# Performance work log

Measured on AMD Instinct MI355X. Metric: run time of the kernel, lower is better.

## Reference

```python
import jax, jax.numpy as jnp
import numpy as np

N, D, B, E, K, H, C = 100000, 256, 20000, 16, 3, 256, 40  # m = K = 3


def setup_inputs() -> dict:
    key = jax.random.key(0)
    ks = jax.random.split(key, 11)
    return {
        "nodes": jax.random.randint(ks[0], (B,), 0, N, dtype=jnp.int32),
        "structure": jax.random.randint(ks[1], (B, E, K), 0, N, dtype=jnp.int32),
        "X": jax.random.normal(ks[2], (N, D), dtype=jnp.float32),
        "beta": jax.random.uniform(ks[3], (1,), dtype=jnp.float32),
        "w_att_w": jax.random.normal(ks[4], (1,), dtype=jnp.float32),
        "w_att_b": jax.random.normal(ks[5], (1,), dtype=jnp.float32),
        "lin_W": jax.random.normal(ks[6], (H, D), dtype=jnp.float32) * 0.05,
        "lin_b": jax.random.normal(ks[7], (H,), dtype=jnp.float32) * 0.05,
        "skip_W": jax.random.normal(ks[8], (H, D), dtype=jnp.float32) * 0.05,
        "cls_W": jax.random.normal(ks[9], (C, H), dtype=jnp.float32) * 0.05,
        "cls_b": jax.random.normal(ks[10], (C,), dtype=jnp.float32) * 0.05,
    }


def reference(nodes, structure, X, beta, w_att_w, w_att_b, lin_W, lin_b, skip_W, cls_W, cls_b):
    # --- TMessagePassing (batched over nodes and hyperedges) ---
    feats = X[structure]                                  # [B, E, K, D] gather
    # variance over nodes in the hyperedge (unbiased=False), mean over feature dim
    edge_var = jnp.var(feats, axis=2).mean(axis=-1)       # [B, E]
    att = jax.nn.sigmoid(w_att_w[0] * edge_var + w_att_b[0])  # [B, E]
    # len(edge) == m (K == m=3): msg = prod(feats[:-1], dim=0)
    msg = jnp.prod(feats[:, :, : K - 1, :], axis=2)       # [B, E, D]
    neigh = jnp.einsum("be,bed->bd", att, msg)            # sum of att * msg over edges
    # --- Encoder (combine == 'sum') ---
    self_feat = X[nodes]                                  # [B, D]
    h = self_feat + neigh
    enc = jax.nn.relu(h @ lin_W.T + lin_b)                # [B, H]
    enc = (1.0 - beta[0]) * enc + beta[0] * (self_feat @ skip_W.T)
    # --- classifier + log_softmax ---
    logits = enc @ cls_W.T + cls_b                        # [B, C]
    return jax.nn.log_softmax(logits, axis=1)
```

## Files before the change

kernel.cpp:

```cpp
#include <hip/hip_runtime.h>
#include <hip/hip_bf16.h>
#include <math.h>

#define Dn 256
#define En 16
#define Kn 3
#define Hn 256
#define Cn 40
#define CnP 48

typedef __attribute__((ext_vector_type(8)))  short bf16x8;
typedef __attribute__((ext_vector_type(4)))  float f32x4;

static __device__ __forceinline__ float bf2f(unsigned short u) {
    return __uint_as_float(((unsigned)u) << 16);
}
static __device__ __forceinline__ unsigned short f2bfbits(float v) {
    __hip_bfloat16 hb = __float2bfloat16(v);
    return *reinterpret_cast<unsigned short*>(&hb);
}
static __device__ __forceinline__ unsigned pack2bf(float a, float b) {
    return (unsigned)f2bfbits(a) | ((unsigned)f2bfbits(b) << 16);
}
static __device__ __forceinline__ unsigned swz4(unsigned boff) {
    return boff ^ (((boff >> 9) & 15u) << 4);
}

__global__ __launch_bounds__(256) void conv_all(
    const float* __restrict__ X, const float* __restrict__ linW,
    const float* __restrict__ skipW, const float* __restrict__ clsW,
    uint4* __restrict__ Xb, uint4* __restrict__ linWp,
    uint4* __restrict__ skipWp, uint4* __restrict__ clsWp,
    int x8, int w8)
{
    int t = blockIdx.x * 256 + threadIdx.x;
    const int c8 = (CnP * Hn) / 8;
    if (t < x8) {
        const float4* iv = reinterpret_cast<const float4*>(X);
        const float4 a = iv[(size_t)t * 2 + 0];
        const float4 b = iv[(size_t)t * 2 + 1];
        Xb[t] = (uint4){pack2bf(a.x, a.y), pack2bf(a.z, a.w),
                        pack2bf(b.x, b.y), pack2bf(b.z, b.w)};
        return;
    }
    t -= x8;
    if (t < w8) {
        const float4* iv = reinterpret_cast<const float4*>(linW);
        const float4 a = iv[(size_t)t * 2 + 0];
        const float4 b = iv[(size_t)t * 2 + 1];
        const int lc = (t >> 5) & 15, ct = t >> 9;
        const int kt = (t >> 2) & 7,  kg = t & 3;
        linWp[(ct * 8 + kt) * 64 + kg * 16 + lc] =
            (uint4){pack2bf(a.x, a.y), pack2bf(a.z, a.w),
                    pack2bf(b.x, b.y), pack2bf(b.z, b.w)};
        return;
    }
    t -= w8;
    if (t < w8) {
        const float4* iv = reinterpret_cast<const float4*>(skipW);
        const float4 a = iv[(size_t)t * 2 + 0];
        const float4 b = iv[(size_t)t * 2 + 1];
        const int lc = (t >> 5) & 15, ct = t >> 9;
        const int kt = (t >> 2) & 7,  kg = t & 3;
        skipWp[(ct * 8 + kt) * 64 + kg * 16 + lc] =
            (uint4){pack2bf(a.x, a.y), pack2bf(a.z, a.w),
                    pack2bf(b.x, b.y), pack2bf(b.z, b.w)};
        return;
    }
    t -= w8;
    if (t < c8) {
        const int col = t >> 5;
        const int lc = col & 15, ct = t >> 9;
        const int kt = (t >> 2) & 7, kg = t & 3;
        const int dst = (ct * 8 + kt) * 64 + kg * 16 + lc;
        if (col < Cn) {
            const float4* iv = reinterpret_cast<const float4*>(clsW);
            const float4 a = iv[(size_t)t * 2 + 0];
            const float4 b = iv[(size_t)t * 2 + 1];
            clsWp[dst] = (uint4){pack2bf(a.x, a.y), pack2bf(a.z, a.w),
                                 pack2bf(b.x, b.y), pack2bf(b.z, b.w)};
        } else {
            clsWp[dst] = (uint4){0u, 0u, 0u, 0u};
        }
    }
}

__global__ __launch_bounds__(256) void mp_kernel_bf(
    const int* __restrict__ nodes, const int* __restrict__ structure,
    const uint2* __restrict__ Xb,
    const float* __restrict__ waw_p, const float* __restrict__ wab_p,
    uint2* __restrict__ h_out, uint2* __restrict__ self_out, int B)
{
    const int wave = threadIdx.x >> 6;
    const int lane = threadIdx.x & 63;
    const int b = blockIdx.x * 4 + wave;
    if (b >= B) return;
    const int ub = __builtin_amdgcn_readfirstlane(b);

    const float waw = waw_p[0];
    const float wab = wab_p[0];

    float4 neigh = make_float4(0.f, 0.f, 0.f, 0.f);
    const int* st = structure + (size_t)ub * (En * Kn);

    #pragma unroll 1
    for (int g = 0; g < En / 4; ++g) {
        int idx[12];
        #pragma unroll
        for (int u = 0; u < 12; ++u) idx[u] = st[g * 12 + u];

        uint2 r0[4], r1[4], r2[4];
        #pragma unroll
        for (int u = 0; u < 4; ++u) {
            r0[u] = Xb[(size_t)idx[u * 3 + 0] * (Dn / 4) + lane];
            r1[u] = Xb[(size_t)idx[u * 3 + 1] * (Dn / 4) + lane];
            r2[u] = Xb[(size_t)idx[u * 3 + 2] * (Dn / 4) + lane];
        }

        float pv[4];
        float4 msg[4];
        #pragma unroll
        for (int u = 0; u < 4; ++u) {
            float4 f0, f1, f2;
            f0.x = bf2f((unsigned short)(r0[u].x & 0xffff));
            f0.y = bf2f((unsigned short)(r0[u].x >> 16));
            f0.z = bf2f((unsigned short)(r0[u].y & 0xffff));
            f0.w = bf2f((unsigned short)(r0[u].y >> 16));
            f1.x = bf2f((unsigned short)(r1[u].x & 0xffff));
            f1.y = bf2f((unsigned short)(r1[u].x >> 16));
            f1.z = bf2f((unsigned short)(r1[u].y & 0xffff));
            f1.w = bf2f((unsigned short)(r1[u].y >> 16));
            f2.x = bf2f((unsigned short)(r2[u].x & 0xffff));
            f2.y = bf2f((unsigned short)(r2[u].x >> 16));
            f2.z = bf2f((unsigned short)(r2[u].y & 0xffff));
            f2.w = bf2f((unsigned short)(r2[u].y >> 16));

            float s2 = 0.f, cr = 0.f, tt;
            s2 = fmaf(f0.x, f0.x, s2); s2 = fmaf(f1.x, f1.x, s2); s2 = fmaf(f2.x, f2.x, s2);
            tt = f1.x + f2.x; cr = fmaf(f0.x, tt, cr); cr = fmaf(f1.x, f2.x, cr);
            s2 = fmaf(f0.y, f0.y, s2); s2 = fmaf(f1.y, f1.y, s2); s2 = fmaf(f2.y, f2.y, s2);
            tt = f1.y + f2.y; cr = fmaf(f0.y, tt, cr); cr = fmaf(f1.y, f2.y, cr);
            s2 = fmaf(f0.z, f0.z, s2); s2 = fmaf(f1.z, f1.z, s2); s2 = fmaf(f2.z, f2.z, s2);
            tt = f1.z + f2.z; cr = fmaf(f0.z, tt, cr); cr = fmaf(f1.z, f2.z, cr);
            s2 = fmaf(f0.w, f0.w, s2); s2 = fmaf(f1.w, f1.w, s2); s2 = fmaf(f2.w, f2.w, s2);
            tt = f1.w + f2.w; cr = fmaf(f0.w, tt, cr); cr = fmaf(f1.w, f2.w, cr);

            pv[u] = s2 - cr;
            msg[u].x = f0.x * f1.x;
            msg[u].y = f0.y * f1.y;
            msg[u].z = f0.z * f1.z;
            msg[u].w = f0.w * f1.w;
        }

        #pragma unroll
        for (int off = 32; off; off >>= 1) {
            #pragma unroll
            for (int u = 0; u < 4; ++u) pv[u] += __shfl_xor(pv[u], off);
        }

        #pragma unroll
        for (int u = 0; u < 4; ++u) {
            const float var_mean = pv[u] * (2.f / (9.f * (float)Dn));
            const float att = 1.f / (1.f + expf(-(waw * var_mean + wab)));
            neigh.x += att * msg[u].x;
            neigh.y += att * msg[u].y;
            neigh.z += att * msg[u].z;
            neigh.w += att * msg[u].w;
        }
    }

    const uint2 sv = Xb[(size_t)nodes[ub] * (Dn / 4) + lane];
    self_out[(size_t)b * (Dn / 4) + lane] = sv;
    const float sx = bf2f((unsigned short)(sv.x & 0xffff));
    const float sy = bf2f((unsigned short)(sv.x >> 16));
    const float sz = bf2f((unsigned short)(sv.y & 0xffff));
    const float sw = bf2f((unsigned short)(sv.y >> 16));
    uint2 o;
    o.x = pack2bf(sx + neigh.x, sy + neigh.y);
    o.y = pack2bf(sz + neigh.z, sw + neigh.w);
    h_out[(size_t)b * (Dn / 4) + lane] = o;
}

__global__ __launch_bounds__(256, 4) void enc_cls16(
    const unsigned short* __restrict__ hB,
    const unsigned short* __restrict__ selfB,
    const uint4* __restrict__ linWp, const float* __restrict__ linb,
    const uint4* __restrict__ skipWp, const float* __restrict__ beta_p,
    const uint4* __restrict__ clsWp,
    const float* __restrict__ clsb,
    float* __restrict__ out, int M)
{
    __shared__ unsigned short hlds[16 * 256];
    __shared__ unsigned short slds[16 * 256];
    __shared__ unsigned short elds[16 * 256];

    const int w    = threadIdx.x >> 6;
    const int l    = threadIdx.x & 63;
    const int lr16 = l & 15;
    const int kg   = l >> 4;
    const int row0 = blockIdx.x * 16;

    #pragma unroll
    for (int it = 0; it < 2; ++it) {
        const int ch = it * 256 + threadIdx.x;
        const int r  = ch >> 5;
        const int c  = ch & 31;
        int grow = row0 + r;
        grow = grow < M ? grow : (M - 1);
        const uint4 hv = *reinterpret_cast<const uint4*>(hB    + (size_t)grow * Dn + c * 8);
        const uint4 sv = *reinterpret_cast<const uint4*>(selfB + (size_t)grow * Dn + c * 8);
        const unsigned boff = swz4((unsigned)(r * 512 + c * 16));
        *reinterpret_cast<uint4*>(reinterpret_cast<char*>(hlds) + boff) = hv;
        *reinterpret_cast<uint4*>(reinterpret_cast<char*>(slds) + boff) = sv;
    }
    __syncthreads();

    f32x4 acc1[4], acc2[4];
    #pragma unroll
    for (int n = 0; n < 4; ++n) {
        acc1[n] = (f32x4){0.f, 0.f, 0.f, 0.f};
        acc2[n] = (f32x4){0.f, 0.f, 0.f, 0.f};
    }

    #pragma unroll 2
    for (int k0 = 0; k0 < Dn; k0 += 32) {
        const int kt = k0 >> 5;
        const unsigned aoff = swz4((unsigned)(lr16 * 512 + k0 * 2 + kg * 16));
        const bf16x8 a1 = *reinterpret_cast<const bf16x8*>(
            reinterpret_cast<const char*>(hlds) + aoff);
        const bf16x8 a2 = *reinterpret_cast<const bf16x8*>(
            reinterpret_cast<const char*>(slds) + aoff);
        #pragma unroll
        for (int n = 0; n < 4; ++n) {
            const int fidx = ((w * 4 + n) * 8 + kt) * 64 + l;
            const bf16x8 b1 = *reinterpret_cast<const bf16x8*>(linWp  + fidx);
            const bf16x8 b2 = *reinterpret_cast<const bf16x8*>(skipWp + fidx);
            acc1[n] = __builtin_amdgcn_mfma_f32_16x16x32_bf16(a1, b1, acc1[n], 0, 0, 0);
            acc2[n] = __builtin_amdgcn_mfma_f32_16x16x32_bf16(a2, b2, acc2[n], 0, 0, 0);
        }
    }

    const float beta = beta_p[0];
    const float omb = 1.f - beta;
    #pragma unroll
    for (int n = 0; n < 4; ++n) {
        const int col = w * 64 + n * 16 + lr16;
        const float bias = linb[col];
        #pragma unroll
        for (int r = 0; r < 4; ++r) {
            const int rowl = kg * 4 + r;
            const float c1 = fmaxf(acc1[n][r] + bias, 0.f);
            const unsigned short v = f2bfbits(omb * c1 + beta * acc2[n][r]);
            const unsigned boff = swz4((unsigned)(rowl * 512 + col * 2));
            *reinterpret_cast<unsigned short*>(
                reinterpret_cast<char*>(elds) + boff) = v;
        }
    }
    __syncthreads();

    if (w == 0) {
        f32x4 cacc[3];
        cacc[0] = (f32x4){0.f,0.f,0.f,0.f};
        cacc[1] = (f32x4){0.f,0.f,0.f,0.f};
        cacc[2] = (f32x4){0.f,0.f,0.f,0.f};

        #pragma unroll
        for (int k0 = 0; k0 < Hn; k0 += 32) {
            const int kt = k0 >> 5;
            const unsigned boff = swz4((unsigned)(lr16 * 512 + k0 * 2 + kg * 16));
            const bf16x8 a = *reinterpret_cast<const bf16x8*>(
                reinterpret_cast<const char*>(elds) + boff);
            #pragma unroll
            for (int t = 0; t < 3; ++t) {
                const bf16x8 bb = *reinterpret_cast<const bf16x8*>(
                    clsWp + ((t * 8 + kt) * 64 + l));
                cacc[t] = __builtin_amdgcn_mfma_f32_16x16x32_bf16(a, bb, cacc[t], 0, 0, 0);
            }
        }

        float bias3[3];
        #pragma unroll
        for (int t = 0; t < 3; ++t) {
            const int cb = t * 16 + lr16;
            bias3[t] = (cb < Cn) ? clsb[cb] : -INFINITY;
        }

        #pragma unroll
        for (int r = 0; r < 4; ++r) {
            float lg0 = cacc[0][r] + bias3[0];
            float lg1 = cacc[1][r] + bias3[1];
            float lg2 = cacc[2][r] + bias3[2];
            float mx = fmaxf(fmaxf(lg0, lg1), lg2);
            #pragma unroll
            for (int off = 8; off; off >>= 1) mx = fmaxf(mx, __shfl_xor(mx, off));
            float se = expf(lg0 - mx) + expf(lg1 - mx) + expf(lg2 - mx);
            #pragma unroll
            for (int off = 8; off; off >>= 1) se += __shfl_xor(se, off);
            const float lse = logf(se);

            const int row = row0 + kg * 4 + r;
            if (row < M) {
                if (lr16 < 8) out[(size_t)row * Cn + 32 + lr16] = lg2 - mx - lse;
                out[(size_t)row * Cn + lr16]      = lg0 - mx - lse;
                out[(size_t)row * Cn + 16 + lr16] = lg1 - mx - lse;
            }
        }
    }
}

__global__ __launch_bounds__(256) void mp_kernel_f32(
    const int* __restrict__ nodes, const int* __restrict__ structure,
    const float* __restrict__ X, const float* __restrict__ waw_p,
    const float* __restrict__ wab_p, float* __restrict__ h_out, int B)
{
    const int wave = threadIdx.x >> 6;
    const int lane = threadIdx.x & 63;
    const int b = blockIdx.x * 4 + wave;
    if (b >= B) return;
    const int ub = __builtin_amdgcn_readfirstlane(b);

    const float waw = waw_p[0];
    const float wab = wab_p[0];
    const float4* __restrict__ Xv = reinterpret_cast<const float4*>(X);

    float4 neigh = make_float4(0.f, 0.f, 0.f, 0.f);
    const int* st = structure + (size_t)ub * (En * Kn);

    #pragma unroll 1
    for (int e = 0; e < En; ++e) {
        const int i0 = st[e * 3 + 0];
        const int i1 = st[e * 3 + 1];
        const int i2 = st[e * 3 + 2];
        const float4 f0 = Xv[(size_t)i0 * (Dn / 4) + lane];
        const float4 f1 = Xv[(size_t)i1 * (Dn / 4) + lane];
        const float4 f2 = Xv[(size_t)i2 * (Dn / 4) + lane];
        float pv = 0.f;
        {
            float a, bb, c, m;
            a = f0.x; bb = f1.x; c = f2.x;
            m = (a + bb + c) * (1.f / 3.f);
            pv += (a * a + bb * bb + c * c) * (1.f / 3.f) - m * m;
            a = f0.y; bb = f1.y; c = f2.y;
            m = (a + bb + c) * (1.f / 3.f);
            pv += (a * a + bb * bb + c * c) * (1.f / 3.f) - m * m;
            a = f0.z; bb = f1.z; c = f2.z;
            m = (a + bb + c) * (1.f / 3.f);
            pv += (a * a + bb * bb + c * c) * (1.f / 3.f) - m * m;
            a = f0.w; bb = f1.w; c = f2.w;
            m = (a + bb + c) * (1.f / 3.f);
            pv += (a * a + bb * bb + c * c) * (1.f / 3.f) - m * m;
        }
        #pragma unroll
        for (int off = 32; off; off >>= 1) pv += __shfl_xor(pv, off);
        const float var_mean = pv * (1.f / (float)Dn);
        const float att = 1.f / (1.f + expf(-(waw * var_mean + wab)));
        neigh.x += att * f0.x * f1.x;
        neigh.y += att * f0.y * f1.y;
        neigh.z += att * f0.z * f1.z;
        neigh.w += att * f0.w * f1.w;
    }

    const float4 s = Xv[(size_t)nodes[ub] * (Dn / 4) + lane];
    float4 h;
    h.x = s.x + neigh.x; h.y = s.y + neigh.y;
    h.z = s.z + neigh.z; h.w = s.w + neigh.w;
    reinterpret_cast<float4*>(h_out)[(size_t)b * (Dn / 4) + lane] = h;
}

#define BM 64
#define BN 64
#define BKs 16
#define LDT 68

__global__ __launch_bounds__(256) void enc_gemm_f32(
    const float* __restrict__ hA, const int* __restrict__ nodes,
    const float* __restrict__ X,
    const float* __restrict__ linW, const float* __restrict__ linb,
    const float* __restrict__ skipW, const float* __restrict__ beta_p,
    float* __restrict__ enc2, int M)
{
    __shared__ float Ats1[BKs][LDT];
    __shared__ float Ats2[BKs][LDT];
    __shared__ float Bts1[BKs][LDT];
    __shared__ float Bts2[BKs][LDT];

    const int tid = threadIdx.x;
    const int tx = tid & 15;
    const int ty = tid >> 4;
    const int row0 = blockIdx.x * BM;
    const int col0 = blockIdx.y * BN;

    const int lr = tid >> 2;
    const int lc = tid & 3;

    const int arow = row0 + lr;
    const bool arow_ok = arow < M;
    const int self_row = arow_ok ? nodes[arow] : 0;

    float acc1[4][4] = {{0.f}}, acc2[4][4] = {{0.f}};

    for (int k0 = 0; k0 < Dn; k0 += BKs) {
        float4 a1v = make_float4(0.f, 0.f, 0.f, 0.f);
        float4 a2v = make_float4(0.f, 0.f, 0.f, 0.f);
        if (arow_ok) {
            a1v = *reinterpret_cast<const float4*>(hA + (size_t)arow * Dn + k0 + lc * 4);
            a2v = *reinterpret_cast<const float4*>(X + (size_t)self_row * Dn + k0 + lc * 4);
        }
        const float4 b1v = *reinterpret_cast<const float4*>(linW + (size_t)(col0 + lr) * Dn + k0 + lc * 4);
        const float4 b2v = *reinterpret_cast<const float4*>(skipW + (size_t)(col0 + lr) * Dn + k0 + lc * 4);

        __syncthreads();
        Ats1[lc * 4 + 0][lr] = a1v.x; Ats1[lc * 4 + 1][lr] = a1v.y;
        Ats1[lc * 4 + 2][lr] = a1v.z; Ats1[lc * 4 + 3][lr] = a1v.w;
        Ats2[lc * 4 + 0][lr] = a2v.x; Ats2[lc * 4 + 1][lr] = a2v.y;
        Ats2[lc * 4 + 2][lr] = a2v.z; Ats2[lc * 4 + 3][lr] = a2v.w;
        Bts1[lc * 4 + 0][lr] = b1v.x; Bts1[lc * 4 + 1][lr] = b1v.y;
        Bts1[lc * 4 + 2][lr] = b1v.z; Bts1[lc * 4 + 3][lr] = b1v.w;
        Bts2[lc * 4 + 0][lr] = b2v.x; Bts2[lc * 4 + 1][lr] = b2v.y;
        Bts2[lc * 4 + 2][lr] = b2v.z; Bts2[lc * 4 + 3][lr] = b2v.w;
        __syncthreads();

        #pragma unroll
        for (int kk = 0; kk < BKs; ++kk) {
            const float4 a1 = *reinterpret_cast<const float4*>(&Ats1[kk][ty * 4]);
            const float4 a2 = *reinterpret_cast<const float4*>(&Ats2[kk][ty * 4]);
            const float4 b1 = *reinterpret_cast<const float4*>(&Bts1[kk][tx * 4]);
            const float4 b2 = *reinterpret_cast<const float4*>(&Bts2[kk][tx * 4]);
            const float a1a[4] = {a1.x, a1.y, a1.z, a1.w};
            const float a2a[4] = {a2.x, a2.y, a2.z, a2.w};
            const float b1a[4] = {b1.x, b1.y, b1.z, b1.w};
            const float b2a[4] = {b2.x, b2.y, b2.z, b2.w};
            #pragma unroll
            for (int i = 0; i < 4; ++i)
                #pragma unroll
                for (int j = 0; j < 4; ++j) {
                    acc1[i][j] = fmaf(a1a[i], b1a[j], acc1[i][j]);
                    acc2[i][j] = fmaf(a2a[i], b2a[j], acc2[i][j]);
                }
        }
    }

    const float beta = beta_p[0];
    const float omb = 1.f - beta;
    #pragma unroll
    for (int i = 0; i < 4; ++i) {
        const int r = row0 + ty * 4 + i;
        if (r >= M) continue;
        #pragma unroll
        for (int j = 0; j < 4; ++j) {
            const int c = col0 + tx * 4 + j;
            float c1 = acc1[i][j] + linb[c];
            c1 = fmaxf(c1, 0.f);
            enc2[(size_t)r * Hn + c] = omb * c1 + beta * acc2[i][j];
        }
    }
}

__global__ __launch_bounds__(256) void cls_kernel_f32(
    const float* __restrict__ enc2, const float* __restrict__ clsW,
    const float* __restrict__ clsb, float* __restrict__ out, int B)
{
    const int wave = threadIdx.x >> 6;
    const int lane = threadIdx.x & 63;
    const int b = blockIdx.x * 4 + wave;
    if (b >= B) return;

    const float4 e = reinterpret_cast<const float4*>(enc2 + (size_t)b * Hn)[lane];
    const float4* __restrict__ clsWv = reinterpret_cast<const float4*>(clsW);

    float mylogit = -INFINITY;
    #pragma unroll
    for (int c0 = 0; c0 < Cn; c0 += 8) {
        float p[8];
        #pragma unroll
        for (int u = 0; u < 8; ++u) {
            const float4 wv = clsWv[(size_t)(c0 + u) * (Hn / 4) + lane];
            p[u] = e.x * wv.x + e.y * wv.y + e.z * wv.z + e.w * wv.w;
        }
        #pragma unroll
        for (int off = 32; off; off >>= 1) {
            #pragma unroll
            for (int u = 0; u < 8; ++u) p[u] += __shfl_xor(p[u], off);
        }
        #pragma unroll
        for (int u = 0; u < 8; ++u)
            if (lane == c0 + u) mylogit = p[u];
    }
    if (lane < Cn) mylogit += clsb[lane];

    float mx = mylogit;
    #pragma unroll
    for (int off = 32; off; off >>= 1) mx = fmaxf(mx, __shfl_xor(mx, off));
    float ex = (lane < Cn) ? expf(mylogit - mx) : 0.f;
    float se = ex;
    #pragma unroll
    for (int off = 32; off; off >>= 1) se += __shfl_xor(se, off);
    const float lse = logf(se);

    if (lane < Cn) out[(size_t)b * Cn + lane] = mylogit - mx - lse;
}

extern "C" void kernel_launch(void* const* d_in, const int* in_sizes, int n_in,
                              void* d_out, int out_size, void* d_ws, size_t ws_size,
                              hipStream_t stream) {
    const int*   nodes     = (const int*)d_in[0];
    const int*   structure = (const int*)d_in[1];
    const float* X         = (const float*)d_in[2];
    const float* beta      = (const float*)d_in[3];
    const float* waw       = (const float*)d_in[4];
    const float* wab       = (const float*)d_in[5];
    const float* linW      = (const float*)d_in[6];
    const float* linb      = (const float*)d_in[7];
    const float* skipW     = (const float*)d_in[8];
    const float* clsW      = (const float*)d_in[9];
    const float* clsb      = (const float*)d_in[10];
    float* out = (float*)d_out;

    const int B = in_sizes[0];
    const int Ntot = in_sizes[2];

    unsigned short* h_bf   = (unsigned short*)d_ws;
    unsigned short* selfb  = h_bf + (size_t)B * Dn;
    unsigned short* Xb     = selfb + (size_t)B * Dn;
    unsigned short* linWp  = Xb + (size_t)Ntot;
    unsigned short* skipWp = linWp + (size_t)Hn * Dn;
    unsigned short* clsWp  = skipWp + (size_t)Hn * Dn;

    const size_t need = ((size_t)B * Dn * 2 + (size_t)Ntot +
                         (size_t)Hn * Dn * 2 + (size_t)CnP * Hn) * 2;

    if (ws_size >= need) {
        const int x8 = Ntot / 8;
        const int w8 = (Hn * Dn) / 8;
        const int c8 = (CnP * Hn) / 8;
        const int G = x8 + 2 * w8 + c8;
        conv_all<<<(G + 255) / 256, 256, 0, stream>>>(
            X, linW, skipW, clsW,
            (uint4*)Xb, (uint4*)linWp, (uint4*)skipWp, (uint4*)clsWp, x8, w8);

        mp_kernel_bf<<<(B + 3) / 4, 256, 0, stream>>>(
            nodes, structure, (const uint2*)Xb, waw, wab,
            (uint2*)h_bf, (uint2*)selfb, B);

        enc_cls16<<<(B + 15) / 16, 256, 0, stream>>>(
            h_bf, selfb, (const uint4*)linWp, linb, (const uint4*)skipWp,
            beta, (const uint4*)clsWp, clsb, out, B);
    } else {
        float* enc2 = (float*)d_ws;
        float* hf   = enc2 + (size_t)B * Hn;
        mp_kernel_f32<<<(B + 3) / 4, 256, 0, stream>>>(nodes, structure, X, waw, wab, hf, B);
        dim3 g2((B + BM - 1) / BM, Hn / BN);
        enc_gemm_f32<<<g2, 256, 0, stream>>>(hf, nodes, X, linW, linb, skipW, beta, enc2, B);
        cls_kernel_f32<<<(B + 3) / 4, 256, 0, stream>>>(enc2, clsW, clsb, out, B);
    }
}
```

Measured before the change: 128.7 us.

## Process 32 rows per block in encoder+classifier kernel to reuse weight fragments

The fused encoder/classifier kernel now handles 32 rows per block instead of 16. Each weight fragment loaded from global memory feeds two MFMA row tiles, which halves weight traffic per row. The encoder output now reuses the h tile's LDS buffer instead of a separate one, with an extra barrier, and two waves compute the classifier instead of one. This doubles accumulator registers, which may pressure occupancy, and the grid now has half as many blocks.

Measured after the change: 120.6 us. 6.3% less time.

```diff
diff --git a/kernel.cpp b/kernel.cpp
--- a/kernel.cpp
+++ b/kernel.cpp
@@ -22,8 +22,8 @@
 static __device__ __forceinline__ unsigned pack2bf(float a, float b) {
     return (unsigned)f2bfbits(a) | ((unsigned)f2bfbits(b) << 16);
 }
-static __device__ __forceinline__ unsigned swz4(unsigned boff) {
-    return boff ^ (((boff >> 9) & 15u) << 4);
+static __device__ __forceinline__ unsigned swz5(unsigned boff) {
+    return boff ^ (((boff >> 9) & 31u) << 4);
 }
 
 __global__ __launch_bounds__(256) void conv_all(
@@ -181,7 +181,7 @@
     h_out[(size_t)b * (Dn / 4) + lane] = o;
 }
 
-__global__ __launch_bounds__(256, 4) void enc_cls16(
+__global__ __launch_bounds__(256, 4) void enc_cls32(
     const unsigned short* __restrict__ hB,
     const unsigned short* __restrict__ selfB,
     const uint4* __restrict__ linWp, const float* __restrict__ linb,
@@ -190,18 +190,17 @@
     const float* __restrict__ clsb,
     float* __restrict__ out, int M)
 {
-    __shared__ unsigned short hlds[16 * 256];
-    __shared__ unsigned short slds[16 * 256];
-    __shared__ unsigned short elds[16 * 256];
+    __shared__ unsigned short hlds[32 * 256];
+    __shared__ unsigned short slds[32 * 256];
 
     const int w    = threadIdx.x >> 6;
     const int l    = threadIdx.x & 63;
     const int lr16 = l & 15;
     const int kg   = l >> 4;
-    const int row0 = blockIdx.x * 16;
-
-    #pragma unroll
-    for (int it = 0; it < 2; ++it) {
+    const int row0 = blockIdx.x * 32;
+
+    #pragma unroll
+    for (int it = 0; it < 4; ++it) {
         const int ch = it * 256 + threadIdx.x;
         const int r  = ch >> 5;
         const int c  = ch & 31;
@@ -209,56 +208,69 @@
         grow = grow < M ? grow : (M - 1);
         const uint4 hv = *reinterpret_cast<const uint4*>(hB    + (size_t)grow * Dn + c * 8);
         const uint4 sv = *reinterpret_cast<const uint4*>(selfB + (size_t)grow * Dn + c * 8);
-        const unsigned boff = swz4((unsigned)(r * 512 + c * 16));
+        const unsigned boff = swz5((unsigned)(r * 512 + c * 16));
         *reinterpret_cast<uint4*>(reinterpret_cast<char*>(hlds) + boff) = hv;
         *reinterpret_cast<uint4*>(reinterpret_cast<char*>(slds) + boff) = sv;
     }
     __syncthreads();
 
-    f32x4 acc1[4], acc2[4];
-    #pragma unroll
-    for (int n = 0; n < 4; ++n) {
-        acc1[n] = (f32x4){0.f, 0.f, 0.f, 0.f};
-        acc2[n] = (f32x4){0.f, 0.f, 0.f, 0.f};
-    }
+    f32x4 acc1[2][4], acc2[2][4];
+    #pragma unroll
+    for (int rt = 0; rt < 2; ++rt)
+        #pragma unroll
+        for (int n = 0; n < 4; ++n) {
+            acc1[rt][n] = (f32x4){0.f, 0.f, 0.f, 0.f};
+            acc2[rt][n] = (f32x4){0.f, 0.f, 0.f, 0.f};
+        }
 
     #pragma unroll 2
     for (int k0 = 0; k0 < Dn; k0 += 32) {
         const int kt = k0 >> 5;
-        const unsigned aoff = swz4((unsigned)(lr16 * 512 + k0 * 2 + kg * 16));
-        const bf16x8 a1 = *reinterpret_cast<const bf16x8*>(
-            reinterpret_cast<const char*>(hlds) + aoff);
-        const bf16x8 a2 = *reinterpret_cast<const bf16x8*>(
-            reinterpret_cast<const char*>(slds) + aoff);
+        bf16x8 a1[2], a2[2];
+        #pragma unroll
+        for (int rt = 0; rt < 2; ++rt) {
+            const unsigned aoff = swz5((unsigned)((rt * 16 + lr16) * 512 + k0 * 2 + kg * 16));
+            a1[rt] = *reinterpret_cast<const bf16x8*>(
+                reinterpret_cast<const char*>(hlds) + aoff);
+            a2[rt] = *reinterpret_cast<const bf16x8*>(
+                reinterpret_cast<const char*>(slds) + aoff);
+        }
         #pragma unroll
         for (int n = 0; n < 4; ++n) {
             const int fidx = ((w * 4 + n) * 8 + kt) * 64 + l;
             const bf16x8 b1 = *reinterpret_cast<const bf16x8*>(linWp  + fidx);
             const bf16x8 b2 = *reinterpret_cast<const bf16x8*>(skipWp + fidx);
-            acc1[n] = __builtin_amdgcn_mfma_f32_16x16x32_bf16(a1, b1, acc1[n], 0, 0, 0);
-            acc2[n] = __builtin_amdgcn_mfma_f32_16x16x32_bf16(a2, b2, acc2[n], 0, 0, 0);
-        }
-    }
+            #pragma unroll
+            for (int rt = 0; rt < 2; ++rt) {
+                acc1[rt][n] = __builtin_amdgcn_mfma_f32_16x16x32_bf16(a1[rt], b1, acc1[rt][n], 0, 0, 0);
+                acc2[rt][n] = __builtin_amdgcn_mfma_f32_16x16x32_bf16(a2[rt], b2, acc2[rt][n], 0, 0, 0);
+            }
+        }
+    }
+    __syncthreads();
 
     const float beta = beta_p[0];
     const float omb = 1.f - beta;
     #pragma unroll
-    for (int n = 0; n < 4; ++n) {
-        const int col = w * 64 + n * 16 + lr16;
-        const float bias = linb[col];
-        #pragma unroll
-        for (int r = 0; r < 4; ++r) {
-            const int rowl = kg * 4 + r;
-            const float c1 = fmaxf(acc1[n][r] + bias, 0.f);
-            const unsigned short v = f2bfbits(omb * c1 + beta * acc2[n][r]);
-            const unsigned boff = swz4((unsigned)(rowl * 512 + col * 2));
-            *reinterpret_cast<unsigned short*>(
-                reinterpret_cast<char*>(elds) + boff) = v;
+    for (int rt = 0; rt < 2; ++rt) {
+        #pragma unroll
+        for (int n = 0; n < 4; ++n) {
+            const int col = w * 64 + n * 16 + lr16;
+            const float bias = linb[col];
+            #pragma unroll
+            for (int r = 0; r < 4; ++r) {
+                const int rowl = rt * 16 + kg * 4 + r;
+                const float c1 = fmaxf(acc1[rt][n][r] + bias, 0.f);
+                const unsigned short v = f2bfbits(omb * c1 + beta * acc2[rt][n][r]);
+                const unsigned boff = swz5((unsigned)(rowl * 512 + col * 2));
+                *reinterpret_cast<unsigned short*>(
+                    reinterpret_cast<char*>(hlds) + boff) = v;
+            }
         }
     }
     __syncthreads();
 
-    if (w == 0) {
+    if (w < 2) {
         f32x4 cacc[3];
         cacc[0] = (f32x4){0.f,0.f,0.f,0.f};
         cacc[1] = (f32x4){0.f,0.f,0.f,0.f};
@@ -267,9 +279,9 @@
         #pragma unroll
         for (int k0 = 0; k0 < Hn; k0 += 32) {
             const int kt = k0 >> 5;
-            const unsigned boff = swz4((unsigned)(lr16 * 512 + k0 * 2 + kg * 16));
+            const unsigned boff = swz5((unsigned)((w * 16 + lr16) * 512 + k0 * 2 + kg * 16));
             const bf16x8 a = *reinterpret_cast<const bf16x8*>(
-                reinterpret_cast<const char*>(elds) + boff);
+                reinterpret_cast<const char*>(hlds) + boff);
             #pragma unroll
             for (int t = 0; t < 3; ++t) {
                 const bf16x8 bb = *reinterpret_cast<const bf16x8*>(
@@ -298,7 +310,7 @@
             for (int off = 8; off; off >>= 1) se += __shfl_xor(se, off);
             const float lse = logf(se);
 
-            const int row = row0 + kg * 4 + r;
+            const int row = row0 + w * 16 + kg * 4 + r;
             if (row < M) {
                 if (lr16 < 8) out[(size_t)row * Cn + 32 + lr16] = lg2 - mx - lse;
                 out[(size_t)row * Cn + lr16]      = lg0 - mx - lse;
@@ -542,7 +554,7 @@
             nodes, structure, (const uint2*)Xb, waw, wab,
             (uint2*)h_bf, (uint2*)selfb, B);
 
-        enc_cls16<<<(B + 15) / 16, 256, 0, stream>>>(
+        enc_cls32<<<(B + 31) / 32, 256, 0, stream>>>(
             h_bf, selfb, (const uint4*)linWp, linb, (const uint4*)skipWp,
             beta, (const uint4*)clsWp, clsb, out, B);
     } else {
```
